# Optimization experiments

Measured on AMD Instinct MI355X. Metric: run time of the kernel, lower is better.

The kernel has to match this reference:

```python
import jax, jax.numpy as jnp
import numpy as np

B, C_IN, N = 8, 512, 4096   # batch, input channels, timesteps
D, K = 256, 2048            # code dim (n_out), codebook size (vq_n_embed)
EMA_G = 0.99                # vq_ema_gamma


def setup_inputs() -> dict:
    key = jax.random.key(0)
    k1, k2, k3 = jax.random.split(key, 3)
    z = jax.random.normal(k1, (B, C_IN, N), jnp.float32)
    # emb: xavier_uniform with gain=10 over (K, D)
    eb = 10.0 * np.sqrt(6.0 / (K + D))
    emb = jax.random.uniform(k2, (K, D), jnp.float32, -eb, eb)
    # 1x1 Conv1d weight (no bias), xavier_uniform over (D, C_IN)
    wb = np.sqrt(6.0 / (D + C_IN))
    W = jax.random.uniform(k3, (D, C_IN), jnp.float32, -wb, wb)
    # EMA buffers as initialized in __init__
    ema_numer = emb * (1.0 - EMA_G)
    ema_denom = jnp.ones((K,), jnp.float32) * (1.0 - EMA_G)
    return {"z": z, "W": W, "emb": emb, "ema_numer": ema_numer, "ema_denom": ema_denom}


def reference(z, W, emb, ema_numer, ema_denom):
    # 1x1 conv (no bias): ze (B, D, N)
    ze = jnp.einsum('dc,bcn->bdn', W, z)
    e = jax.lax.stop_gradient(emb)  # sg(emb)
    # Squared L2 distances (B, K, N) via ||ze||^2 + ||e||^2 - 2 e.ze
    # (mathematically equal to the broadcasted (ze-e)^2 sum, without the
    #  huge (B,K,D,N) intermediate)
    ze_sq = jnp.sum(ze * ze, axis=1)              # (B, N)
    e_sq = jnp.sum(e * e, axis=1)                 # (K,)
    cross = jnp.einsum('kd,bdn->bkn', e, ze)      # (B, K, N)
    d2 = ze_sq[:, None, :] + e_sq[None, :, None] - 2.0 * cross
    min_ind = jnp.argmin(d2, axis=1)              # (B, N) int
    zq = jnp.take(e, min_ind, axis=0).transpose(0, 2, 1)  # (B, D, N)
    # ReplaceGrad straight-through: value = zq, gradient flows to ze
    out = ze + jax.lax.stop_gradient(zq - ze)
    # EMA codebook statistics (scatter-add over assignments)
    flat_ind = min_ind.reshape(-1)                          # (B*N,)
    flat_ze = ze.transpose(0, 2, 1).reshape(-1, D)          # (B*N, D)
    z_sum = jax.ops.segment_sum(flat_ze, flat_ind, num_segments=K)
    n_sum = jax.ops.segment_sum(jnp.ones((flat_ind.shape[0],), ze.dtype), flat_ind, num_segments=K)
    ema_numer_new = EMA_G * ema_numer + (1.0 - EMA_G) * z_sum
    ema_denom_new = EMA_G * ema_denom + (1.0 - EMA_G) * n_sum
    return out, ema_numer_new, ema_denom_new
```

## Files before the change

### kernel.cpp

```cpp
#include <hip/hip_runtime.h>

#define B_   8
#define CIN  512
#define NN_  4096
#define DD   256
#define KK   2048
#define KSPLIT 4
#define KPER (KK / KSPLIT)
#define NG   (B_ * NN_)

typedef _Float16 f16x8 __attribute__((ext_vector_type(8)));
typedef _Float16 f16x4 __attribute__((ext_vector_type(4)));
typedef float    f32x16 __attribute__((ext_vector_type(16)));

#define MFMA16 __builtin_amdgcn_mfma_f32_32x32x16_f16

#define GLDS16(gp, lp) __builtin_amdgcn_global_load_lds( \
    (const __attribute__((address_space(1))) void*)(gp), \
    (__attribute__((address_space(3))) void*)(lp), 16, 0, 0)

__device__ __forceinline__ unsigned ford(float f) {
  unsigned u = __float_as_uint(f);
  return (u & 0x80000000u) ? ~u : (u | 0x80000000u);
}

__global__ __launch_bounds__(256) void k_init0(const float* __restrict__ emb,
                                               const float* __restrict__ ema_numer,
                                               float* __restrict__ esq,
                                               _Float16* __restrict__ emb_h,
                                               _Float16* __restrict__ emb_l,
                                               float* __restrict__ out_numer,
                                               unsigned* __restrict__ mind64w,
                                               int* __restrict__ hist,
                                               int* __restrict__ done) {
  const int bid = blockIdx.x;
  const int t = threadIdx.x;
  if (bid < KK / 4) {
    int lane = t & 63;
    int k = bid * 4 + (t >> 6);
    float4 v = *(const float4*)&emb[(size_t)k * DD + 4 * lane];
    float s = v.x * v.x + v.y * v.y + v.z * v.z + v.w * v.w;
    f16x4 h, l;
    float* vp = (float*)&v;
#pragma unroll
    for (int i = 0; i < 4; i++) {
      _Float16 hh = (_Float16)vp[i];
      h[i] = hh;
      l[i] = (_Float16)(vp[i] - (float)hh);
    }
    *(f16x4*)&emb_h[(size_t)k * DD + 4 * lane] = h;
    *(f16x4*)&emb_l[(size_t)k * DD + 4 * lane] = l;
    for (int off = 32; off > 0; off >>= 1) s += __shfl_down(s, off, 64);
    if (lane == 0) esq[k] = s;
  } else {
    int i = (bid - KK / 4) * 256 + t;
    if (i < KK * DD) out_numer[i] = 0.99f * ema_numer[i];
    else {
      int j = i - KK * DD;
      if (j < 2 * NG) mind64w[j] = 0xFFFFFFFFu;
      else if (j < 2 * NG + KK) hist[j - 2 * NG] = 0;
      else done[j - 2 * NG - KK] = 0;
    }
  }
}

__global__ __launch_bounds__(256) void k_ze(const float* __restrict__ W,
                                            const float* __restrict__ z,
                                            _Float16* __restrict__ zeT_h,
                                            _Float16* __restrict__ zeT_l) {
  __shared__ __align__(16) char sm[69632];
  const int t = threadIdx.x;
  const int w = t >> 6, lane = t & 63;
  const int lr = lane & 31, lh = lane >> 5;
  const int wm = w & 1, wn = w >> 1;
  const int swz = (lr >> 1) & 3;
  const int b = blockIdx.z, d0 = blockIdx.y * 128, n0 = blockIdx.x * 128;

  auto stageA = [&](int buf, int c0) {
    _Float16* Ah = (_Float16*)(sm + buf * 8192);
    _Float16* Al = (_Float16*)(sm + 16384 + buf * 8192);
#pragma unroll
    for (int i = 0; i < 4; i++) {
      int fid = i * 256 + t;
      int d = fid >> 3, q8 = fid & 7;
      float4 v = *(const float4*)&W[(size_t)(d0 + d) * CIN + c0 + 4 * q8];
      float* vp = (float*)&v;
      f16x4 h, l;
#pragma unroll
      for (int e = 0; e < 4; e++) {
        _Float16 hh = (_Float16)vp[e];
        h[e] = hh;
        l[e] = (_Float16)(vp[e] - (float)hh);
      }
      int p16 = (q8 >> 1) ^ ((d >> 1) & 3);
      int off = d * 32 + p16 * 8 + (q8 & 1) * 4;
      *(f16x4*)&Ah[off] = h;
      *(f16x4*)&Al[off] = l;
    }
  };

  auto stageZ = [&](int buf, int c0) {
    const int n_l = t & 127, cg = t >> 7;
    const float* gp = z + ((size_t)b * CIN + c0 + cg * 16) * NN_ + n0 + n_l;
    float v[16];
#pragma unroll
    for (int j = 0; j < 16; j++) v[j] = gp[(size_t)j * NN_];
    _Float16* Zh = (_Float16*)(sm + 32768 + buf * 8192);
    _Float16* Zl = (_Float16*)(sm + 49152 + buf * 8192);
#pragma unroll
    for (int q = 0; q < 2; q++) {
      f16x8 h, l;
#pragma unroll
      for (int e = 0; e < 8; e++) {
        float x = v[q * 8 + e];
        _Float16 hh = (_Float16)x;
        h[e] = hh;
        l[e] = (_Float16)(x - (float)hh);
      }
      int p = (cg * 2 + q) ^ ((n_l >> 1) & 3);
      *(f16x8*)&Zh[n_l * 32 + p * 8] = h;
      *(f16x8*)&Zl[n_l * 32 + p * 8] = l;
    }
  };

  f32x16 acc[2][2];
#pragma unroll
  for (int mt = 0; mt < 2; mt++)
#pragma unroll
    for (int nt = 0; nt < 2; nt++)
#pragma unroll
      for (int i = 0; i < 16; i++) acc[mt][nt][i] = 0.0f;

  stageA(0, 0);
  stageZ(0, 0);
  int buf = 0;
  for (int c0 = 0; c0 < CIN; c0 += 32) {
    __syncthreads();
    if (c0 + 32 < CIN) { stageA(buf ^ 1, c0 + 32); stageZ(buf ^ 1, c0 + 32); }
    const _Float16* WhB = (const _Float16*)(sm + buf * 8192);
    const _Float16* WlB = (const _Float16*)(sm + 16384 + buf * 8192);
    const _Float16* ZhB = (const _Float16*)(sm + 32768 + buf * 8192);
    const _Float16* ZlB = (const _Float16*)(sm + 49152 + buf * 8192);
#pragma unroll
    for (int s = 0; s < 2; s++) {
      const int p = (2 * s + lh) ^ swz;
      const int acol = p * 8;
      const int ar0 = (wm * 64 + lr) * 32 + acol;
      const int ar1 = (wm * 64 + 32 + lr) * 32 + acol;
      const int br0 = (wn * 64 + lr) * 32 + acol;
      const int br1 = (wn * 64 + 32 + lr) * 32 + acol;
      f16x8 ah0 = *(const f16x8*)(WhB + ar0);
      f16x8 ah1 = *(const f16x8*)(WhB + ar1);
      f16x8 al0 = *(const f16x8*)(WlB + ar0);
      f16x8 al1 = *(const f16x8*)(WlB + ar1);
      f16x8 bh0 = *(const f16x8*)(ZhB + br0);
      f16x8 bh1 = *(const f16x8*)(ZhB + br1);
      f16x8 bl0 = *(const f16x8*)(ZlB + br0);
      f16x8 bl1 = *(const f16x8*)(ZlB + br1);
      acc[0][0] = MFMA16(ah0, bh0, acc[0][0], 0, 0, 0);
      acc[0][1] = MFMA16(ah0, bh1, acc[0][1], 0, 0, 0);
      acc[1][0] = MFMA16(ah1, bh0, acc[1][0], 0, 0, 0);
      acc[1][1] = MFMA16(ah1, bh1, acc[1][1], 0, 0, 0);
      acc[0][0] = MFMA16(ah0, bl0, acc[0][0], 0, 0, 0);
      acc[0][1] = MFMA16(ah0, bl1, acc[0][1], 0, 0, 0);
      acc[1][0] = MFMA16(ah1, bl0, acc[1][0], 0, 0, 0);
      acc[1][1] = MFMA16(ah1, bl1, acc[1][1], 0, 0, 0);
      acc[0][0] = MFMA16(al0, bh0, acc[0][0], 0, 0, 0);
      acc[0][1] = MFMA16(al0, bh1, acc[0][1], 0, 0, 0);
      acc[1][0] = MFMA16(al1, bh0, acc[1][0], 0, 0, 0);
      acc[1][1] = MFMA16(al1, bh1, acc[1][1], 0, 0, 0);
    }
    buf ^= 1;
  }

  __syncthreads();
  _Float16* Eh = (_Float16*)sm;
  _Float16* El = (_Float16*)(sm + 33792);
#pragma unroll
  for (int mt = 0; mt < 2; mt++)
#pragma unroll
    for (int nt = 0; nt < 2; nt++) {
      int n_l = wn * 64 + nt * 32 + lr;
#pragma unroll
      for (int g = 0; g < 4; g++) {
        int d_l = wm * 64 + mt * 32 + 8 * g + 4 * lh;
        f16x4 h, l;
#pragma unroll
        for (int e = 0; e < 4; e++) {
          float x = acc[mt][nt][4 * g + e];
          _Float16 hh = (_Float16)x;
          h[e] = hh;
          l[e] = (_Float16)(x - (float)hh);
        }
        *(f16x4*)&Eh[n_l * 132 + d_l] = h;
        *(f16x4*)&El[n_l * 132 + d_l] = l;
      }
    }
  __syncthreads();
  _Float16* gh = zeT_h + ((size_t)b * NN_ + n0) * DD + d0;
  _Float16* gl = zeT_l + ((size_t)b * NN_ + n0) * DD + d0;
#pragma unroll
  for (int i = 0; i < 16; i++) {
    int n = i * 8 + w * 2 + lh;
    int d = 4 * lr;
    *(f16x4*)&gh[(size_t)n * DD + d] = *(const f16x4*)&Eh[n * 132 + d];
    *(f16x4*)&gl[(size_t)n * DD + d] = *(const f16x4*)&El[n * 132 + d];
  }
}

__global__ __launch_bounds__(256) void k_argmin(const _Float16* __restrict__ emb_h,
                                                const _Float16* __restrict__ emb_l,
                                                const _Float16* __restrict__ zeT_h,
                                                const _Float16* __restrict__ zeT_l,
                                                const float* __restrict__ esq,
                                                unsigned long long* __restrict__ mind64) {
  __shared__ __align__(16) char sm[69632];
  const int t = threadIdx.x;
  const int w = t >> 6, lane = t & 63;
  const int lr = lane & 31, lh = lane >> 5;
  const int wm = w & 1, wn = w >> 1;
  const int swz = (lr >> 1) & 3;
  const int b = blockIdx.y, n0 = blockIdx.x * 128, ks = blockIdx.z;
  const int kbase = ks * KPER;

  float* esqs = (float*)(sm + 65536);
  *(float2*)&esqs[2 * t] = *(const float2*)&esq[kbase + 2 * t];

  const _Float16* zb_h = zeT_h + ((size_t)b * NN_ + n0) * DD;
  const _Float16* zb_l = zeT_l + ((size_t)b * NN_ + n0) * DD;

  auto stage = [&](int buf, int kt, int dc) {
    const int k0 = kbase + kt * 128;
    const int q = lane & 3, rr = lane >> 2;
    const int g = q ^ ((rr >> 1) & 3);
    const int rb0 = 32 * w;
#pragma unroll
    for (int j = 0; j < 2; j++) {
      int rb = rb0 + 16 * j;
      int r = rb + rr;
      int col = dc + 8 * g;
      size_t eo = (size_t)(k0 + r) * DD + col;
      size_t zo = (size_t)r * DD + col;
      char* lb = sm + (size_t)buf * 8192 + rb * 64;
      GLDS16(emb_h + eo, lb);
      GLDS16(emb_l + eo, lb + 16384);
      GLDS16(zb_h + zo, lb + 32768);
      GLDS16(zb_l + zo, lb + 49152);
    }
  };

  f32x16 vzero;
#pragma unroll
  for (int i = 0; i < 16; i++) vzero[i] = 0.0f;

  float bestv[2];
  int   besti[2];
  bestv[0] = bestv[1] = 3.4e38f;
  besti[0] = besti[1] = 0;

  stage(0, 0, 0);
  int buf = 0;
  for (int kt = 0; kt < 4; kt++) {
    f32x16 acc00 = vzero, acc01 = vzero, acc10 = vzero, acc11 = vzero;
    for (int dc = 0; dc < DD; dc += 32) {
      __syncthreads();
      if (dc + 32 < DD) stage(buf ^ 1, kt, dc + 32);
      else if (kt < 3) stage(buf ^ 1, kt + 1, 0);
      const _Float16* EHb = (const _Float16*)(sm + buf * 8192);
      const _Float16* ELb = (const _Float16*)(sm + 16384 + buf * 8192);
      const _Float16* ZHb = (const _Float16*)(sm + 32768 + buf * 8192);
      const _Float16* ZLb = (const _Float16*)(sm + 49152 + buf * 8192);
#pragma unroll
      for (int s = 0; s < 2; s++) {
        const int p = (2 * s + lh) ^ swz;
        const int acol = p * 8;
        const int ar0 = (wm * 64 + lr) * 32 + acol;
        const int ar1 = (wm * 64 + 32 + lr) * 32 + acol;
        const int br0 = (wn * 64 + lr) * 32 + acol;
        const int br1 = (wn * 64 + 32 + lr) * 32 + acol;
        f16x8 ah0 = *(const f16x8*)(EHb + ar0);
        f16x8 ah1 = *(const f16x8*)(EHb + ar1);
        f16x8 al0 = *(const f16x8*)(ELb + ar0);
        f16x8 al1 = *(const f16x8*)(ELb + ar1);
        f16x8 bh0 = *(const f16x8*)(ZHb + br0);
        f16x8 bh1 = *(const f16x8*)(ZHb + br1);
        f16x8 bl0 = *(const f16x8*)(ZLb + br0);
        f16x8 bl1 = *(const f16x8*)(ZLb + br1);
        acc00 = MFMA16(ah0, bh0, acc00, 0, 0, 0);
        acc01 = MFMA16(ah0, bh1, acc01, 0, 0, 0);
        acc10 = MFMA16(ah1, bh0, acc10, 0, 0, 0);
        acc11 = MFMA16(ah1, bh1, acc11, 0, 0, 0);
        acc00 = MFMA16(ah0, bl0, acc00, 0, 0, 0);
        acc01 = MFMA16(ah0, bl1, acc01, 0, 0, 0);
        acc10 = MFMA16(ah1, bl0, acc10, 0, 0, 0);
        acc11 = MFMA16(ah1, bl1, acc11, 0, 0, 0);
        acc00 = MFMA16(al0, bh0, acc00, 0, 0, 0);
        acc01 = MFMA16(al0, bh1, acc01, 0, 0, 0);
        acc10 = MFMA16(al1, bh0, acc10, 0, 0, 0);
        acc11 = MFMA16(al1, bh1, acc11, 0, 0, 0);
      }
      buf ^= 1;
    }
#pragma unroll
    for (int mt = 0; mt < 2; mt++)
#pragma unroll
      for (int nt = 0; nt < 2; nt++) {
        const f32x16& a = (mt == 0) ? (nt == 0 ? acc00 : acc01)
                                    : (nt == 0 ? acc10 : acc11);
#pragma unroll
        for (int r = 0; r < 16; r++) {
          int kl = kt * 128 + wm * 64 + mt * 32 + (r & 3) + 8 * (r >> 2) + 4 * lh;
          float d2 = esqs[kl] - 2.0f * a[r];
          int kg = kbase + kl;
          if (d2 < bestv[nt] || (d2 == bestv[nt] && kg < besti[nt])) {
            bestv[nt] = d2; besti[nt] = kg;
          }
        }
      }
  }

#pragma unroll
  for (int nt = 0; nt < 2; nt++) {
    float ov = __shfl_xor(bestv[nt], 32, 64);
    int   oi = __shfl_xor(besti[nt], 32, 64);
    if (ov < bestv[nt] || (ov == bestv[nt] && oi < besti[nt])) {
      bestv[nt] = ov; besti[nt] = oi;
    }
  }
  float* pv = (float*)(sm + 67584);
  int*   pi = (int*)(sm + 68608);
  __syncthreads();
  if (lh == 0) {
#pragma unroll
    for (int nt = 0; nt < 2; nt++) {
      pv[(w * 2 + nt) * 32 + lr] = bestv[nt];
      pi[(w * 2 + nt) * 32 + lr] = besti[nt];
    }
  }
  __syncthreads();
  if (t < 128) {
    int wn2 = t >> 6, nt = (t >> 5) & 1, nl = t & 31;
    int i0 = ((2 * wn2 + 0) * 2 + nt) * 32 + nl;
    int i1 = ((2 * wn2 + 1) * 2 + nt) * 32 + nl;
    float v0 = pv[i0], v1 = pv[i1];
    int   j0 = pi[i0], j1 = pi[i1];
    if (v1 < v0 || (v1 == v0 && j1 < j0)) { v0 = v1; j0 = j1; }
    unsigned long long pk = ((unsigned long long)ford(v0) << 32) | (unsigned)j0;
    atomicMin(&mind64[(size_t)b * NN_ + n0 + t], pk);
  }
}

__global__ __launch_bounds__(256) void k_scan(const unsigned long long* __restrict__ mind64,
                                              const float* __restrict__ ema_denom,
                                              int* __restrict__ hist,
                                              int* __restrict__ done,
                                              int* __restrict__ cursor,
                                              float* __restrict__ out_denom) {
  __shared__ int h[KK];
  __shared__ int ps[256];
  __shared__ int lastFlag;
  const int t = threadIdx.x;
#pragma unroll
  for (int i = 0; i < 8; i++) h[t + 256 * i] = 0;
  __syncthreads();
  const int base = blockIdx.x * (NG / 16);
#pragma unroll
  for (int i = 0; i < NG / 16 / 256; i++) {
    int idx = (int)(mind64[base + i * 256 + t] & 0xFFFFFFFFULL);
    atomicAdd(&h[idx], 1);
  }
  __syncthreads();
#pragma unroll
  for (int i = 0; i < 8; i++) {
    int v = h[t + 256 * i];
    if (v) atomicAdd(&hist[t + 256 * i], v);
  }
  __threadfence();
  __syncthreads();
  if (t == 0) lastFlag = (atomicAdd(done, 1) == 15);
  __syncthreads();
  if (!lastFlag) return;

  int c[8], s = 0;
#pragma unroll
  for (int e = 0; e < 8; e++) { c[e] = atomicAdd(&hist[8 * t + e], 0); s += c[e]; }
  ps[t] = s;
  __syncthreads();
  for (int off = 1; off < 256; off <<= 1) {
    int v = (t >= off) ? ps[t - off] : 0;
    __syncthreads();
    ps[t] += v;
    __syncthreads();
  }
  int run = ps[t] - s;
#pragma unroll
  for (int e = 0; e < 8; e++) {
    cursor[8 * t + e] = run;
    out_denom[8 * t + e] = 0.99f * ema_denom[8 * t + e]
                         + 0.009999999776482582f * (float)c[e];
    run += c[e];
  }
}

__global__ __launch_bounds__(256) void k_out(const float* __restrict__ emb,
                                             const unsigned long long* __restrict__ mind64,
                                             float* __restrict__ out,
                                             int* __restrict__ cursor,
                                             int* __restrict__ sortp) {
  __shared__ __align__(16) float E[64][257];
  __shared__ int idxl[64];
  const int t = threadIdx.x;
  const int b  = blockIdx.y;
  const int n0 = blockIdx.x * 64;
  if (t < 64) idxl[t] = (int)(mind64[(size_t)b * NN_ + n0 + t] & 0xFFFFFFFFULL);
  __syncthreads();

  if (t < 64) {
    int g = b * NN_ + n0 + t;
    int k = idxl[t];
    int p = atomicAdd(&cursor[k], 1);
    sortp[p] = (k << 15) | g;
  }

  for (int i = 0; i < 16; i++) {
    int cid = t + 256 * i;
    int r = cid >> 6, q = cid & 63;
    float4 v = *(const float4*)&emb[(size_t)idxl[r] * DD + 4 * q];
    float* vp = (float*)&v;
    E[r][4 * q + 0] = vp[0];
    E[r][4 * q + 1] = vp[1];
    E[r][4 * q + 2] = vp[2];
    E[r][4 * q + 3] = vp[3];
  }
  __syncthreads();
  const int nq = t & 15, dg = t >> 4;
  float* outb = out + (size_t)b * DD * NN_ + n0;
#pragma unroll
  for (int i = 0; i < 16; i++) {
    int d = i * 16 + dg;
    float4 v = make_float4(E[4 * nq + 0][d], E[4 * nq + 1][d],
                           E[4 * nq + 2][d], E[4 * nq + 3][d]);
    *(float4*)&outb[(size_t)d * NN_ + 4 * nq] = v;
  }
}

__global__ __launch_bounds__(256) void k_zsum(const int* __restrict__ sortp,
                                              const _Float16* __restrict__ zeT_h,
                                              const _Float16* __restrict__ zeT_l,
                                              float* __restrict__ out_numer) {
  const float OG = 0.009999999776482582f;
  __shared__ int sg[128];
  const int t = threadIdx.x;
  const int w = t >> 6, lane = t & 63;
  if (t < 128) sg[t] = sortp[blockIdx.x * 128 + t];
  __syncthreads();
  const int base = w * 32;
  float acc[4] = {0.f, 0.f, 0.f, 0.f};
  int cur = sg[base] >> 15;
  for (int j = 0; j < 32; j++) {
    int e = sg[base + j];
    int k = e >> 15, g = e & 32767;
    if (k != cur) {
      float* zs = &out_numer[(size_t)cur * DD + 4 * lane];
#pragma unroll
      for (int x = 0; x < 4; x++) { atomicAdd(&zs[x], OG * acc[x]); acc[x] = 0.f; }
      cur = k;
    }
    f16x4 h = *(const f16x4*)&zeT_h[(size_t)g * DD + 4 * lane];
    f16x4 l = *(const f16x4*)&zeT_l[(size_t)g * DD + 4 * lane];
#pragma unroll
    for (int x = 0; x < 4; x++) acc[x] += (float)h[x] + (float)l[x];
  }
  float* zs = &out_numer[(size_t)cur * DD + 4 * lane];
#pragma unroll
  for (int x = 0; x < 4; x++) atomicAdd(&zs[x], OG * acc[x]);
}

extern "C" void kernel_launch(void* const* d_in, const int* in_sizes, int n_in,
                              void* d_out, int out_size, void* d_ws, size_t ws_size,
                              hipStream_t stream) {
  (void)in_sizes; (void)n_in; (void)out_size; (void)ws_size;
  const float* z         = (const float*)d_in[0];
  const float* W         = (const float*)d_in[1];
  const float* emb       = (const float*)d_in[2];
  const float* ema_numer = (const float*)d_in[3];
  const float* ema_denom = (const float*)d_in[4];

  float* out       = (float*)d_out;
  float* out_numer = out + (size_t)B_ * DD * NN_;
  float* out_denom = out_numer + (size_t)KK * DD;

  const size_t ZET = (size_t)B_ * NN_ * DD;
  _Float16* zeT_h = (_Float16*)d_ws;
  _Float16* zeT_l = zeT_h + ZET;
  float* esq    = (float*)(zeT_l + ZET);
  int*   cursor = (int*)(esq + KK);
  int*   sortp  = cursor + KK;
  unsigned long long* mind64 = (unsigned long long*)(sortp + NG);
  int*   hist   = (int*)(mind64 + NG);
  int*   done   = hist + KK;
  _Float16* emb_h = (_Float16*)(done + 256);
  _Float16* emb_l = emb_h + (size_t)KK * DD;

  const int initBlocks = KK / 4 + (KK * DD + 2 * NG + KK + 256) / 256;
  k_init0<<<dim3(initBlocks), 256, 0, stream>>>(emb, ema_numer, esq, emb_h, emb_l,
                                                out_numer, (unsigned*)mind64, hist, done);
  k_ze<<<dim3(NN_ / 128, DD / 128, B_), 256, 0, stream>>>(W, z, zeT_h, zeT_l);
  k_argmin<<<dim3(NN_ / 128, B_, KSPLIT), 256, 0, stream>>>(emb_h, emb_l, zeT_h, zeT_l,
                                                            esq, mind64);
  k_scan<<<dim3(16), 256, 0, stream>>>(mind64, ema_denom, hist, done, cursor, out_denom);
  k_out<<<dim3(NN_ / 64, B_), 256, 0, stream>>>(emb, mind64, out, cursor, sortp);
  k_zsum<<<dim3(NG / 128), 256, 0, stream>>>(sortp, zeT_h, zeT_l, out_numer);
}
```

Measured before the change: 285.8 us.

## Load ze B-operand directly from global into registers instead of LDS staging

The ze (B operand) tiles in the argmin GEMM are no longer staged through LDS. Each wave now loads its B fragments straight from global memory into registers, prefetching the next chunk after the current MFMAs. Shared memory drops from about 68KB to about 36KB, which may allow more blocks per CU and removes LDS bandwidth and bank pressure for B. In exchange, the B loads are uncoalesced per-lane 16-byte reads, and waves that share the same ze rows fetch them redundantly through cache.

Result: slower. 309.2 us (+8.2%).

```diff
diff --git a/kernel.cpp b/kernel.cpp
--- a/kernel.cpp
+++ b/kernel.cpp
@@ -214,7 +214,7 @@
                                                 const _Float16* __restrict__ zeT_l,
                                                 const float* __restrict__ esq,
                                                 unsigned long long* __restrict__ mind64) {
-  __shared__ __align__(16) char sm[69632];
+  __shared__ __align__(16) char sm[36864];
   const int t = threadIdx.x;
   const int w = t >> 6, lane = t & 63;
   const int lr = lane & 31, lh = lane >> 5;
@@ -223,7 +223,7 @@
   const int b = blockIdx.y, n0 = blockIdx.x * 128, ks = blockIdx.z;
   const int kbase = ks * KPER;
 
-  float* esqs = (float*)(sm + 65536);
+  float* esqs = (float*)(sm + 32768);
   *(float2*)&esqs[2 * t] = *(const float2*)&esq[kbase + 2 * t];
 
   const _Float16* zb_h = zeT_h + ((size_t)b * NN_ + n0) * DD;
@@ -240,12 +240,23 @@
       int r = rb + rr;
       int col = dc + 8 * g;
       size_t eo = (size_t)(k0 + r) * DD + col;
-      size_t zo = (size_t)r * DD + col;
       char* lb = sm + (size_t)buf * 8192 + rb * 64;
       GLDS16(emb_h + eo, lb);
       GLDS16(emb_l + eo, lb + 16384);
-      GLDS16(zb_h + zo, lb + 32768);
-      GLDS16(zb_l + zo, lb + 49152);
+    }
+  };
+
+  f16x8 rbh0[2], rbh1[2], rbl0[2], rbl1[2];
+  const size_t zr0 = (size_t)(wn * 64 + lr) * DD;
+  const size_t zr1 = (size_t)(wn * 64 + 32 + lr) * DD;
+  auto loadB = [&](int dc2) {
+#pragma unroll
+    for (int s = 0; s < 2; s++) {
+      int col = dc2 + 16 * s + 8 * lh;
+      rbh0[s] = *(const f16x8*)(zb_h + zr0 + col);
+      rbh1[s] = *(const f16x8*)(zb_h + zr1 + col);
+      rbl0[s] = *(const f16x8*)(zb_l + zr0 + col);
+      rbl1[s] = *(const f16x8*)(zb_l + zr1 + col);
     }
   };
 
@@ -259,6 +270,7 @@
   besti[0] = besti[1] = 0;
 
   stage(0, 0, 0);
+  loadB(0);
   int buf = 0;
   for (int kt = 0; kt < 4; kt++) {
     f32x16 acc00 = vzero, acc01 = vzero, acc10 = vzero, acc11 = vzero;
@@ -268,36 +280,32 @@
       else if (kt < 3) stage(buf ^ 1, kt + 1, 0);
       const _Float16* EHb = (const _Float16*)(sm + buf * 8192);
       const _Float16* ELb = (const _Float16*)(sm + 16384 + buf * 8192);
-      const _Float16* ZHb = (const _Float16*)(sm + 32768 + buf * 8192);
-      const _Float16* ZLb = (const _Float16*)(sm + 49152 + buf * 8192);
 #pragma unroll
       for (int s = 0; s < 2; s++) {
         const int p = (2 * s + lh) ^ swz;
         const int acol = p * 8;
         const int ar0 = (wm * 64 + lr) * 32 + acol;
         const int ar1 = (wm * 64 + 32 + lr) * 32 + acol;
-        const int br0 = (wn * 64 + lr) * 32 + acol;
-        const int br1 = (wn * 64 + 32 + lr) * 32 + acol;
         f16x8 ah0 = *(const f16x8*)(EHb + ar0);
         f16x8 ah1 = *(const f16x8*)(EHb + ar1);
         f16x8 al0 = *(const f16x8*)(ELb + ar0);
         f16x8 al1 = *(const f16x8*)(ELb + ar1);
-        f16x8 bh0 = *(const f16x8*)(ZHb + br0);
-        f16x8 bh1 = *(const f16x8*)(ZHb + br1);
-        f16x8 bl0 = *(const f16x8*)(ZLb + br0);
-        f16x8 bl1 = *(const f16x8*)(ZLb + br1);
-        acc00 = MFMA16(ah0, bh0, acc00, 0, 0, 0);
-        acc01 = MFMA16(ah0, bh1, acc01, 0, 0, 0);
-        acc10 = MFMA16(ah1, bh0, acc10, 0, 0, 0);
-        acc11 = MFMA16(ah1, bh1, acc11, 0, 0, 0);
-        acc00 = MFMA16(ah0, bl0, acc00, 0, 0, 0);
-        acc01 = MFMA16(ah0, bl1, acc01, 0, 0, 0);
-        acc10 = MFMA16(ah1, bl0, acc10, 0, 0, 0);
-        acc11 = MFMA16(ah1, bl1, acc11, 0, 0, 0);
-        acc00 = MFMA16(al0, bh0, acc00, 0, 0, 0);
-        acc01 = MFMA16(al0, bh1, acc01, 0, 0, 0);
-        acc10 = MFMA16(al1, bh0, acc10, 0, 0, 0);
-        acc11 = MFMA16(al1, bh1, acc11, 0, 0, 0);
+        acc00 = MFMA16(ah0, rbh0[s], acc00, 0, 0, 0);
+        acc01 = MFMA16(ah0, rbh1[s], acc01, 0, 0, 0);
+        acc10 = MFMA16(ah1, rbh0[s], acc10, 0, 0, 0);
+        acc11 = MFMA16(ah1, rbh1[s], acc11, 0, 0, 0);
+        acc00 = MFMA16(ah0, rbl0[s], acc00, 0, 0, 0);
+        acc01 = MFMA16(ah0, rbl1[s], acc01, 0, 0, 0);
+        acc10 = MFMA16(ah1, rbl0[s], acc10, 0, 0, 0);
+        acc11 = MFMA16(ah1, rbl1[s], acc11, 0, 0, 0);
+        acc00 = MFMA16(al0, rbh0[s], acc00, 0, 0, 0);
+        acc01 = MFMA16(al0, rbh1[s], acc01, 0, 0, 0);
+        acc10 = MFMA16(al1, rbh0[s], acc10, 0, 0, 0);
+        acc11 = MFMA16(al1, rbh1[s], acc11, 0, 0, 0);
+      }
+      if (!(kt == 3 && dc + 32 >= DD)) {
+        int ndc = (dc + 32 < DD) ? dc + 32 : 0;
+        loadB(ndc);
       }
       buf ^= 1;
     }
@@ -327,8 +335,8 @@
       bestv[nt] = ov; besti[nt] = oi;
     }
   }
-  float* pv = (float*)(sm + 67584);
-  int*   pi = (int*)(sm + 68608);
+  float* pv = (float*)(sm + 34816);
+  int*   pi = (int*)(sm + 35840);
   __syncthreads();
   if (lh == 0) {
 #pragma unroll
```
